# Kernel optimization log

Measured on AMD Instinct MI355X. Metric: run time of the kernel, lower is better.

Reference implementation:

```python
import jax, jax.numpy as jnp
import numpy as np

C = 256
D = C // 8  # query/key channels


def setup_inputs() -> dict:
    key = jax.random.key(0)
    ks = jax.random.split(key, 7)
    x = jax.random.normal(ks[0], (4, C, 64, 64), dtype=jnp.float32)
    s1 = 1.0 / np.sqrt(C)
    w1 = jax.random.normal(ks[1], (D, C), dtype=jnp.float32) * s1
    b1 = jax.random.normal(ks[2], (D,), dtype=jnp.float32) * 0.01
    w2 = jax.random.normal(ks[3], (D, C), dtype=jnp.float32) * s1
    b2 = jax.random.normal(ks[4], (D,), dtype=jnp.float32) * 0.01
    w3 = jax.random.normal(ks[5], (C, C), dtype=jnp.float32) * s1
    b3 = jax.random.normal(ks[6], (C,), dtype=jnp.float32) * 0.01
    return {"x": x, "w1": w1, "b1": b1, "w2": w2, "b2": b2, "w3": w3, "b3": b3}


def reference(x, w1, b1, w2, b2, w3, b3):
    B, Cc, W, H = x.shape
    N = W * H
    xf = x.reshape(B, Cc, N)  # [B, C, N] flattened spatial
    # 1x1 convs are per-pixel linear maps over channels
    q = jnp.einsum('dc,bcn->bnd', w1, xf) + b1  # [B, N, D]
    k = jnp.einsum('dc,bcn->bdn', w2, xf) + b2[:, None]  # [B, D, N]
    v = jnp.einsum('oc,bcn->bon', w3, xf) + b3[:, None]  # [B, C, N]
    energy = jnp.einsum('bnd,bdm->bnm', q, k)  # [B, N, N]
    attn = jax.nn.softmax(energy, axis=-1)
    out = jnp.einsum('bcm,bnm->bcn', v, attn)  # bmm(V, attn^T)
    out = out.reshape(B, Cc, W, H) + x
    return out
```

## Files before the change

### kernel.cpp

```cpp
#include <hip/hip_runtime.h>
#include <hip/hip_fp16.h>

typedef _Float16 half8 __attribute__((ext_vector_type(8)));
typedef _Float16 half2v __attribute__((ext_vector_type(2)));
typedef float f32x16 __attribute__((ext_vector_type(16)));
typedef float f32x4v __attribute__((ext_vector_type(4)));

#define MFMA16(A, B, C) __builtin_amdgcn_mfma_f32_32x32x16_f16((A), (B), (C), 0, 0, 0)

__device__ __forceinline__ f32x16 fzero16() {
  f32x16 z;
#pragma unroll
  for (int i = 0; i < 16; ++i) z[i] = 0.0f;
  return z;
}

__global__ __launch_bounds__(256) void wprep_kernel(
    const float* __restrict__ w1, const float* __restrict__ w2,
    const float* __restrict__ w3,
    _Float16* __restrict__ w1p, _Float16* __restrict__ w2p,
    _Float16* __restrict__ w3p)
{
  const int t = threadIdx.x;
  const int blk = blockIdx.x;
  if (blk < 8) {
    const int cot = blk;
    for (int e = t; e < 8192; e += 256) {
      const int j = e & 7, l = (e >> 3) & 63, cs = e >> 9;
      const int lr = l & 31, h = l >> 5;
      const int row = cot * 32 + lr;
      const int col = cs * 16 + 4 * h + (j & 3) + 8 * (j >> 2);
      w3p[((cot * 16 + cs) * 64 + l) * 8 + j] = (_Float16)w3[row * 256 + col];
    }
  } else {
    for (int e = t; e < 8192; e += 256) {
      const int j = e & 7, l = (e >> 3) & 63, cs = e >> 9;
      const int lr = l & 31, h = l >> 5;
      const int col = cs * 16 + 4 * h + (j & 3) + 8 * (j >> 2);
      const int idx = (cs * 64 + l) * 8 + j;
      w1p[idx] = (_Float16)w1[lr * 256 + col];
      w2p[idx] = (_Float16)w2[lr * 256 + col];
    }
  }
}

__global__ __launch_bounds__(256) void qkv_proj_kernel(
    const float* __restrict__ x,
    const _Float16* __restrict__ w1p, const float* __restrict__ b1,
    const _Float16* __restrict__ w2p, const float* __restrict__ b2,
    const _Float16* __restrict__ w3p, const float* __restrict__ b3,
    _Float16* __restrict__ qb, _Float16* __restrict__ kb,
    _Float16* __restrict__ vb)
{
  __shared__ f32x4v red[4][2][4][64];
  const int t = threadIdx.x, w = t >> 6, l = t & 63;
  const int lr = l & 31, h = l >> 5;
  const int b = blockIdx.x >> 7;
  const int nt = blockIdx.x & 127;
  const float* xb = x + (size_t)b * 256 * 4096 + nt * 32 + lr;
  const int cot0 = w * 2, cot1 = w * 2 + 1;

  f32x16 accq = fzero16(), acck = fzero16();
  f32x16 accv0 = fzero16(), accv1 = fzero16();

  for (int cs = 0; cs < 16; ++cs) {
    const int c0 = cs * 16 + 4 * h;
    half8 xh;
#pragma unroll
    for (int j = 0; j < 8; ++j) {
      const int c = c0 + (j & 3) + 8 * (j >> 2);
      xh[j] = (_Float16)xb[(size_t)c * 4096];
    }
    const half8 wh0 = *(const half8*)&w3p[((cot0 * 16 + cs) * 64 + l) * 8];
    const half8 wh1 = *(const half8*)&w3p[((cot1 * 16 + cs) * 64 + l) * 8];
    accv0 = MFMA16(xh, wh0, accv0);
    accv1 = MFMA16(xh, wh1, accv1);
    if ((cs >> 2) == w) {
      const half8 w1h = *(const half8*)&w1p[(cs * 64 + l) * 8];
      const half8 w2h = *(const half8*)&w2p[(cs * 64 + l) * 8];
      accq = MFMA16(w1h, xh, accq);
      acck = MFMA16(w2h, xh, acck);
    }
  }

  const float bv0 = b3[cot0 * 32 + lr];
  const float bv1 = b3[cot1 * 32 + lr];
#pragma unroll
  for (int hfq = 0; hfq < 2; ++hfq) {
    half8 p0, p1;
#pragma unroll
    for (int j = 0; j < 8; ++j) {
      p0[j] = (_Float16)(accv0[8 * hfq + j] + bv0);
      p1[j] = (_Float16)(accv1[8 * hfq + j] + bv1);
    }
    const int ms = nt * 2 + hfq;
    *(half8*)&vb[((((size_t)b * 256 + ms) * 8 + cot0) * 64 + l) * 8] = p0;
    *(half8*)&vb[((((size_t)b * 256 + ms) * 8 + cot1) * 64 + l) * 8] = p1;
  }

#pragma unroll
  for (int i4 = 0; i4 < 4; ++i4) {
    f32x4v q4, k4;
#pragma unroll
    for (int c = 0; c < 4; ++c) { q4[c] = accq[4 * i4 + c]; k4[c] = acck[4 * i4 + c]; }
    red[w][0][i4][l] = q4;
    red[w][1][i4][l] = k4;
  }
  __syncthreads();
  if (w < 2) {
    _Float16* dst = (w == 0) ? qb : kb;
    const float* bias = (w == 0) ? b1 : b2;
    f32x16 tot;
#pragma unroll
    for (int i4 = 0; i4 < 4; ++i4) {
      f32x4v v = red[0][w][i4][l];
      v += red[1][w][i4][l];
      v += red[2][w][i4][l];
      v += red[3][w][i4][l];
#pragma unroll
      for (int c = 0; c < 4; ++c) tot[4 * i4 + c] = v[c];
    }
#pragma unroll
    for (int ds = 0; ds < 2; ++ds) {
      half8 ph;
#pragma unroll
      for (int j = 0; j < 8; ++j) {
        const int d = 16 * ds + 4 * h + (j & 3) + 8 * (j >> 2);
        ph[j] = (_Float16)(tot[8 * ds + j] + bias[d]);
      }
      *(half8*)&dst[((((size_t)b * 128 + nt) * 2 + ds) * 64 + l) * 8] = ph;
    }
  }
}

__device__ __forceinline__ float max16(float vm, const f32x16& s) {
  const float g1 = fmaxf(fmaxf(s[0], s[1]), s[2]);
  const float g2 = fmaxf(fmaxf(s[3], s[4]), s[5]);
  const float g3 = fmaxf(fmaxf(s[6], s[7]), s[8]);
  const float g4 = fmaxf(fmaxf(s[9], s[10]), s[11]);
  const float g5 = fmaxf(fmaxf(s[12], s[13]), s[14]);
  const float h1 = fmaxf(fmaxf(g1, g2), g3);
  const float h2 = fmaxf(fmaxf(g4, g5), s[15]);
  return fmaxf(fmaxf(vm, h1), h2);
}

__global__ __launch_bounds__(512) void rowmax_kernel(
    const _Float16* __restrict__ qb, const _Float16* __restrict__ kb,
    float* __restrict__ Mrow)
{
  __shared__ float red[2][8][32];
  const int t = threadIdx.x, w = t >> 6, l = t & 63;
  const int bid = blockIdx.x;
  const int xcd = bid & 7;
  const int b = xcd >> 1;
  const int sp = ((bid >> 3) << 1) | (xcd & 1);
  const int sl0 = sp * 2, sl1 = sp * 2 + 1;
  const _Float16* qp0 = qb + ((((size_t)b * 128 + sl0) * 2) * 64 + l) * 8;
  const _Float16* qp1 = qb + ((((size_t)b * 128 + sl1) * 2) * 64 + l) * 8;
  const half8 q00 = *(const half8*)qp0;
  const half8 q01 = *(const half8*)(qp0 + 512);
  const half8 q10 = *(const half8*)qp1;
  const half8 q11 = *(const half8*)(qp1 + 512);
  float vm0 = -3.0e38f, vm1 = -3.0e38f;
  for (int mt = w * 16; mt < w * 16 + 16; ++mt) {
    const _Float16* kp = kb + ((((size_t)b * 128 + mt) * 2) * 64 + l) * 8;
    const half8 k0 = *(const half8*)kp;
    const half8 k1 = *(const half8*)(kp + 512);
    f32x16 s0 = fzero16();
    s0 = MFMA16(k0, q00, s0);
    s0 = MFMA16(k1, q01, s0);
    f32x16 s1 = fzero16();
    s1 = MFMA16(k0, q10, s1);
    s1 = MFMA16(k1, q11, s1);
    vm0 = max16(vm0, s0);
    vm1 = max16(vm1, s1);
  }
  vm0 = fmaxf(vm0, __shfl_xor(vm0, 32));
  vm1 = fmaxf(vm1, __shfl_xor(vm1, 32));
  if (l < 32) { red[0][w][l] = vm0; red[1][w][l] = vm1; }
  __syncthreads();
  if (t < 64) {
    const int slab = t >> 5, r = t & 31;
    float m = red[slab][0][r];
#pragma unroll
    for (int ww = 1; ww < 8; ++ww) m = fmaxf(m, red[slab][ww][r]);
    Mrow[(size_t)b * 4096 + (sp * 2 + slab) * 32 + r] = m;
  }
}

__global__ __launch_bounds__(512, 1) void attn_kernel(
    const _Float16* __restrict__ qb, const _Float16* __restrict__ kb,
    const _Float16* __restrict__ vb, const float* __restrict__ Mrow,
    const float* __restrict__ x, float* __restrict__ out)
{
  __shared__ __align__(16) _Float16 Plds[2][2][2][8][64][8];
  __shared__ float Lred[2][4][32];
  const int t = threadIdx.x, w = t >> 6, l = t & 63;
  const int lr = l & 31, h = l >> 5;
  const int bid = blockIdx.x;
  const int xcd = bid & 7;
  const int b = xcd >> 1;
  const int rg = ((bid >> 3) << 1) | (xcd & 1);
  const int sw = w >> 2;
  const int kq = w & 3;

  const _Float16* kbase = kb + (size_t)b * 131072 + (size_t)l * 8;
  const _Float16* vbase = vb + (size_t)b * 1048576 + (size_t)w * 512 + (size_t)l * 8;

#define KF(kt, ds) (*(const half8*)(kbase + ((size_t)(((kt) * 4 + kq) * 2 + (ds))) * 512))
#define VF(kt, ks) (*(const half8*)(vbase + ((size_t)(((kt) * 8 + (ks)) * 8)) * 512))

  const int rt32q = rg * 2 + sw;
  const _Float16* qp = qb + (((size_t)b * 128 + rt32q) * 2 * 64 + l) * 8;
  const half8 qf0 = *(const half8*)qp;
  const half8 qf1 = *(const half8*)(qp + 512);
  const float LOG2E = 1.44269504088896340736f;
  const float Mr = Mrow[(size_t)b * 4096 + rt32q * 32 + lr];
  const float nM2 = -Mr * LOG2E;

  f32x16 acc0 = fzero16(), acc1 = fzero16();
  float Lacc = 0.f;
  half8 va0[8], va1[8];
  half8 ka0, ka1, kb0_, kb1_;

#define EXPPACK(S, BUF, TI)                                                    \
  {                                                                            \
    float pvv[16];                                                             \
    float ls = 0.f;                                                            \
    _Pragma("unroll") for (int i = 0; i < 16; ++i) {                           \
      pvv[i] = exp2f(fmaf((S)[i], LOG2E, nM2)); ls += pvv[i];                  \
    }                                                                          \
    Lacc += ls;                                                                \
    union { half8 v; half2v h2[4]; } u0, u1;                                   \
    _Pragma("unroll") for (int jj = 0; jj < 4; ++jj) {                         \
      auto a0 = __builtin_amdgcn_cvt_pkrtz(pvv[2 * jj], pvv[2 * jj + 1]);      \
      auto a1 = __builtin_amdgcn_cvt_pkrtz(pvv[8 + 2 * jj], pvv[8 + 2 * jj + 1]); \
      u0.h2[jj] = *(half2v*)&a0;                                               \
      u1.h2[jj] = *(half2v*)&a1;                                               \
    }                                                                          \
    *(half8*)&Plds[BUF][TI][sw][kq * 2 + 0][l][0] = u0.v;                      \
    *(half8*)&Plds[BUF][TI][sw][kq * 2 + 1][l][0] = u1.v;                      \
  }

#define PVC(CB, TI, VA)                                                        \
  {                                                                            \
    __builtin_amdgcn_s_setprio(1);                                             \
    _Pragma("unroll") for (int ks = 0; ks < 8; ++ks) {                         \
      const half8 pb0 = *(const half8*)&Plds[CB][TI][0][ks][l][0];             \
      const half8 pb1 = *(const half8*)&Plds[CB][TI][1][ks][l][0];             \
      acc0 = MFMA16(VA[ks], pb0, acc0);                                        \
      acc1 = MFMA16(VA[ks], pb1, acc1);                                        \
    }                                                                          \
    __builtin_amdgcn_s_setprio(0);                                             \
  }

#pragma unroll
  for (int ks = 0; ks < 8; ++ks) va0[ks] = VF(0, ks);
#pragma unroll
  for (int ks = 0; ks < 8; ++ks) va1[ks] = VF(1, ks);
  {
    const half8 k00 = KF(0, 0), k01 = KF(0, 1);
    f32x16 s = fzero16();
    s = MFMA16(k00, qf0, s);
    s = MFMA16(k01, qf1, s);
    ka0 = KF(2, 0); ka1 = KF(2, 1);
    EXPPACK(s, 0, 0)
  }
  {
    const half8 k10 = KF(1, 0), k11 = KF(1, 1);
    f32x16 s = fzero16();
    s = MFMA16(k10, qf0, s);
    s = MFMA16(k11, qf1, s);
    kb0_ = KF(3, 0); kb1_ = KF(3, 1);
    EXPPACK(s, 0, 1)
  }
  asm volatile("s_waitcnt lgkmcnt(0)" ::: "memory");
  __builtin_amdgcn_s_barrier();
  asm volatile("" ::: "memory");

  for (int P = 0; P < 16; ++P) {
    const int CB = P & 1, PB = CB ^ 1;
    const int p0 = 2 * P + 2, p1 = 2 * P + 3;

    if (p0 < 32) {
      f32x16 s = fzero16();
      s = MFMA16(ka0, qf0, s);
      s = MFMA16(ka1, qf1, s);
      if (p0 + 2 < 32) { ka0 = KF(p0 + 2, 0); ka1 = KF(p0 + 2, 1); }
      EXPPACK(s, PB, 0)
    }
    PVC(CB, 0, va0)
    if (p0 < 32) {
#pragma unroll
      for (int ks = 0; ks < 8; ++ks) va0[ks] = VF(p0, ks);
    }

    if (p1 < 32) {
      f32x16 s = fzero16();
      s = MFMA16(kb0_, qf0, s);
      s = MFMA16(kb1_, qf1, s);
      if (p1 + 2 < 32) { kb0_ = KF(p1 + 2, 0); kb1_ = KF(p1 + 2, 1); }
      EXPPACK(s, PB, 1)
    }
    PVC(CB, 1, va1)
    if (p1 < 32) {
#pragma unroll
      for (int ks = 0; ks < 8; ++ks) va1[ks] = VF(p1, ks);
    }

    asm volatile("s_waitcnt lgkmcnt(0)" ::: "memory");
    __builtin_amdgcn_s_barrier();
    asm volatile("" ::: "memory");
  }
#undef PVC
#undef EXPPACK
#undef KF
#undef VF

  {
    const float l2 = Lacc + __shfl_xor(Lacc, 32);
    if (l < 32) Lred[sw][kq][lr] = l2;
  }
  __syncthreads();
  const float invL0 = 1.0f / (Lred[0][0][lr] + Lred[0][1][lr] + Lred[0][2][lr] + Lred[0][3][lr]);
  const float invL1 = 1.0f / (Lred[1][0][lr] + Lred[1][1][lr] + Lred[1][2][lr] + Lred[1][3][lr]);

  const float* xb = x + (size_t)b * 1048576;
  float* ob = out + (size_t)b * 1048576;
  const int nn0 = rg * 64 + lr;
  const int nn1 = rg * 64 + 32 + lr;
#pragma unroll
  for (int reg = 0; reg < 16; ++reg) {
    const int crel = (reg & 3) + 8 * (reg >> 2) + 4 * h;
    const int cout = w * 32 + crel;
    const size_t o0 = (size_t)cout * 4096 + nn0;
    ob[o0] = acc0[reg] * invL0 + xb[o0];
    const size_t o1 = (size_t)cout * 4096 + nn1;
    ob[o1] = acc1[reg] * invL1 + xb[o1];
  }
}

extern "C" void kernel_launch(void* const* d_in, const int* in_sizes, int n_in,
                              void* d_out, int out_size, void* d_ws, size_t ws_size,
                              hipStream_t stream) {
  const float* x  = (const float*)d_in[0];
  const float* w1 = (const float*)d_in[1];
  const float* b1 = (const float*)d_in[2];
  const float* w2 = (const float*)d_in[3];
  const float* b2 = (const float*)d_in[4];
  const float* w3 = (const float*)d_in[5];
  const float* b3 = (const float*)d_in[6];
  float* out = (float*)d_out;

  char* ws = (char*)d_ws;
  _Float16* qb  = (_Float16*)(ws);
  _Float16* kb  = (_Float16*)(ws + (1u << 20));
  _Float16* vb  = (_Float16*)(ws + (2u << 20));
  float*    Mrow = (float*)(ws + (10u << 20));
  _Float16* w1p = (_Float16*)(ws + (10u << 20) + (64u << 10));
  _Float16* w2p = (_Float16*)(ws + (10u << 20) + (96u << 10));
  _Float16* w3p = (_Float16*)(ws + (10u << 20) + (128u << 10));

  hipLaunchKernelGGL(wprep_kernel, dim3(9), dim3(256), 0, stream,
                     w1, w2, w3, w1p, w2p, w3p);
  hipLaunchKernelGGL(qkv_proj_kernel, dim3(512), dim3(256), 0, stream,
                     x, w1p, b1, w2p, b2, w3p, b3, qb, kb, vb);
  hipLaunchKernelGGL(rowmax_kernel, dim3(256), dim3(512), 0, stream, qb, kb, Mrow);
  hipLaunchKernelGGL(attn_kernel, dim3(256), dim3(512), 0, stream,
                     qb, kb, vb, Mrow, x, out);
}
```

Baseline: 74.21 us.

## Split PV key tiles across wave groups with 64-channel waves and LDS reduction

Each wave now computes 64 output channels on half of the key tiles (selected by wave group g) instead of 32 channels on every key tile. This halves the LDS reads of P per MFMA, because each P fragment feeds two channel blocks. The two partial accumulators are then summed through LDS before the final normalisation and residual add. In exchange it doubles the V register buffers and accumulators, which raises VGPR pressure, and adds an extra LDS reduction and barrier in the epilogue.

```diff
diff --git a/kernel.cpp b/kernel.cpp
--- a/kernel.cpp
+++ b/kernel.cpp
@@ -201,16 +201,17 @@
   const int xcd = bid & 7;
   const int b = xcd >> 1;
   const int rg = ((bid >> 3) << 1) | (xcd & 1);
-  const int sw = w >> 2;
+  const int g = w >> 2;
   const int kq = w & 3;
+  const int c2 = w & 3;
 
   const _Float16* kbase = kb + (size_t)b * 131072 + (size_t)l * 8;
-  const _Float16* vbase = vb + (size_t)b * 1048576 + (size_t)w * 512 + (size_t)l * 8;
+  const _Float16* vbase = vb + (size_t)b * 1048576 + (size_t)(c2 * 2) * 512 + (size_t)l * 8;
 
 #define KF(kt, ds) (*(const half8*)(kbase + ((size_t)(((kt) * 4 + kq) * 2 + (ds))) * 512))
-#define VF(kt, ks) (*(const half8*)(vbase + ((size_t)(((kt) * 8 + (ks)) * 8)) * 512))
-
-  const int rt32q = rg * 2 + sw;
+#define VF(kt, ks, ci) (*(const half8*)(vbase + ((size_t)(((kt) * 8 + (ks)) * 8 + (ci))) * 512))
+
+  const int rt32q = rg * 2 + g;
   const _Float16* qp = qb + (((size_t)b * 128 + rt32q) * 2 * 64 + l) * 8;
   const half8 qf0 = *(const half8*)qp;
   const half8 qf1 = *(const half8*)(qp + 512);
@@ -218,9 +219,9 @@
   const float Mr = Mrow[(size_t)b * 4096 + rt32q * 32 + lr];
   const float nM2 = -Mr * LOG2E;
 
-  f32x16 acc0 = fzero16(), acc1 = fzero16();
+  f32x16 a00 = fzero16(), a01 = fzero16(), a10 = fzero16(), a11 = fzero16();
   float Lacc = 0.f;
-  half8 va0[8], va1[8];
+  half8 vA[16], vB[16];
   half8 ka0, ka1, kb0_, kb1_;
 
 #define EXPPACK(S, BUF, TI)                                                    \
@@ -233,31 +234,62 @@
     Lacc += ls;                                                                \
     union { half8 v; half2v h2[4]; } u0, u1;                                   \
     _Pragma("unroll") for (int jj = 0; jj < 4; ++jj) {                         \
-      auto a0 = __builtin_amdgcn_cvt_pkrtz(pvv[2 * jj], pvv[2 * jj + 1]);      \
-      auto a1 = __builtin_amdgcn_cvt_pkrtz(pvv[8 + 2 * jj], pvv[8 + 2 * jj + 1]); \
-      u0.h2[jj] = *(half2v*)&a0;                                               \
-      u1.h2[jj] = *(half2v*)&a1;                                               \
-    }                                                                          \
-    *(half8*)&Plds[BUF][TI][sw][kq * 2 + 0][l][0] = u0.v;                      \
-    *(half8*)&Plds[BUF][TI][sw][kq * 2 + 1][l][0] = u1.v;                      \
-  }
-
-#define PVC(CB, TI, VA)                                                        \
+      auto q0 = __builtin_amdgcn_cvt_pkrtz(pvv[2 * jj], pvv[2 * jj + 1]);      \
+      auto q1 = __builtin_amdgcn_cvt_pkrtz(pvv[8 + 2 * jj], pvv[8 + 2 * jj + 1]); \
+      u0.h2[jj] = *(half2v*)&q0;                                               \
+      u1.h2[jj] = *(half2v*)&q1;                                               \
+    }                                                                          \
+    *(half8*)&Plds[BUF][TI][g][kq * 2 + 0][l][0] = u0.v;                       \
+    *(half8*)&Plds[BUF][TI][g][kq * 2 + 1][l][0] = u1.v;                       \
+  }
+
+#define PVC(CB, VA)                                                            \
   {                                                                            \
     __builtin_amdgcn_s_setprio(1);                                             \
     _Pragma("unroll") for (int ks = 0; ks < 8; ++ks) {                         \
-      const half8 pb0 = *(const half8*)&Plds[CB][TI][0][ks][l][0];             \
-      const half8 pb1 = *(const half8*)&Plds[CB][TI][1][ks][l][0];             \
-      acc0 = MFMA16(VA[ks], pb0, acc0);                                        \
-      acc1 = MFMA16(VA[ks], pb1, acc1);                                        \
+      const half8 pb0 = *(const half8*)&Plds[CB][g][0][ks][l][0];              \
+      const half8 pb1 = *(const half8*)&Plds[CB][g][1][ks][l][0];              \
+      a00 = MFMA16(VA[ks], pb0, a00);                                          \
+      a01 = MFMA16(VA[8 + ks], pb0, a01);                                      \
+      a10 = MFMA16(VA[ks], pb1, a10);                                          \
+      a11 = MFMA16(VA[8 + ks], pb1, a11);                                      \
     }                                                                          \
     __builtin_amdgcn_s_setprio(0);                                             \
   }
 
-#pragma unroll
-  for (int ks = 0; ks < 8; ++ks) va0[ks] = VF(0, ks);
-#pragma unroll
-  for (int ks = 0; ks < 8; ++ks) va1[ks] = VF(1, ks);
+#define BODY(P, VC, VN)                                                        \
+  {                                                                            \
+    const int CBv = (P) & 1, PBv = CBv ^ 1;                                    \
+    const int Tv = 2 * (P) + g;                                                \
+    const int p0 = 2 * (P) + 2, p1 = 2 * (P) + 3;                              \
+    if (Tv + 2 < 32) {                                                         \
+      _Pragma("unroll") for (int ks = 0; ks < 8; ++ks) {                       \
+        VN[ks] = VF(Tv + 2, ks, 0);                                            \
+        VN[8 + ks] = VF(Tv + 2, ks, 1);                                        \
+      }                                                                        \
+    }                                                                          \
+    if (p0 < 32) {                                                             \
+      f32x16 s = fzero16();                                                    \
+      s = MFMA16(ka0, qf0, s);                                                 \
+      s = MFMA16(ka1, qf1, s);                                                 \
+      if (p0 + 2 < 32) { ka0 = KF(p0 + 2, 0); ka1 = KF(p0 + 2, 1); }           \
+      EXPPACK(s, PBv, 0)                                                       \
+    }                                                                          \
+    PVC(CBv, VC)                                                               \
+    if (p1 < 32) {                                                             \
+      f32x16 s = fzero16();                                                    \
+      s = MFMA16(kb0_, qf0, s);                                                \
+      s = MFMA16(kb1_, qf1, s);                                                \
+      if (p1 + 2 < 32) { kb0_ = KF(p1 + 2, 0); kb1_ = KF(p1 + 2, 1); }         \
+      EXPPACK(s, PBv, 1)                                                       \
+    }                                                                          \
+    asm volatile("s_waitcnt lgkmcnt(0)" ::: "memory");                         \
+    __builtin_amdgcn_s_barrier();                                              \
+    asm volatile("" ::: "memory");                                             \
+  }
+
+#pragma unroll
+  for (int ks = 0; ks < 8; ++ks) { vA[ks] = VF(g, ks, 0); vA[8 + ks] = VF(g, ks, 1); }
   {
     const half8 k00 = KF(0, 0), k01 = KF(0, 1);
     f32x16 s = fzero16();
@@ -278,40 +310,11 @@
   __builtin_amdgcn_s_barrier();
   asm volatile("" ::: "memory");
 
-  for (int P = 0; P < 16; ++P) {
-    const int CB = P & 1, PB = CB ^ 1;
-    const int p0 = 2 * P + 2, p1 = 2 * P + 3;
-
-    if (p0 < 32) {
-      f32x16 s = fzero16();
-      s = MFMA16(ka0, qf0, s);
-      s = MFMA16(ka1, qf1, s);
-      if (p0 + 2 < 32) { ka0 = KF(p0 + 2, 0); ka1 = KF(p0 + 2, 1); }
-      EXPPACK(s, PB, 0)
-    }
-    PVC(CB, 0, va0)
-    if (p0 < 32) {
-#pragma unroll
-      for (int ks = 0; ks < 8; ++ks) va0[ks] = VF(p0, ks);
-    }
-
-    if (p1 < 32) {
-      f32x16 s = fzero16();
-      s = MFMA16(kb0_, qf0, s);
-      s = MFMA16(kb1_, qf1, s);
-      if (p1 + 2 < 32) { kb0_ = KF(p1 + 2, 0); kb1_ = KF(p1 + 2, 1); }
-      EXPPACK(s, PB, 1)
-    }
-    PVC(CB, 1, va1)
-    if (p1 < 32) {
-#pragma unroll
-      for (int ks = 0; ks < 8; ++ks) va1[ks] = VF(p1, ks);
-    }
-
-    asm volatile("s_waitcnt lgkmcnt(0)" ::: "memory");
-    __builtin_amdgcn_s_barrier();
-    asm volatile("" ::: "memory");
-  }
+  for (int PP = 0; PP < 16; PP += 2) {
+    BODY(PP, vA, vB)
+    BODY(PP + 1, vB, vA)
+  }
+#undef BODY
 #undef PVC
 #undef EXPPACK
 #undef KF
@@ -319,24 +322,51 @@
 
   {
     const float l2 = Lacc + __shfl_xor(Lacc, 32);
-    if (l < 32) Lred[sw][kq][lr] = l2;
+    if (l < 32) Lred[g][kq][lr] = l2;
   }
   __syncthreads();
-  const float invL0 = 1.0f / (Lred[0][0][lr] + Lred[0][1][lr] + Lred[0][2][lr] + Lred[0][3][lr]);
-  const float invL1 = 1.0f / (Lred[1][0][lr] + Lred[1][1][lr] + Lred[1][2][lr] + Lred[1][3][lr]);
-
-  const float* xb = x + (size_t)b * 1048576;
-  float* ob = out + (size_t)b * 1048576;
-  const int nn0 = rg * 64 + lr;
-  const int nn1 = rg * 64 + 32 + lr;
-#pragma unroll
-  for (int reg = 0; reg < 16; ++reg) {
-    const int crel = (reg & 3) + 8 * (reg >> 2) + 4 * h;
-    const int cout = w * 32 + crel;
-    const size_t o0 = (size_t)cout * 4096 + nn0;
-    ob[o0] = acc0[reg] * invL0 + xb[o0];
-    const size_t o1 = (size_t)cout * 4096 + nn1;
-    ob[o1] = acc1[reg] * invL1 + xb[o1];
+
+  float* fl = (float*)&Plds[0][0][0][0][0][0];
+  if (g == 0) {
+#pragma unroll
+    for (int j = 0; j < 4; ++j) {
+      const f32x16 av = (j == 0) ? a00 : (j == 1) ? a01 : (j == 2) ? a10 : a11;
+#pragma unroll
+      for (int reg = 0; reg < 16; ++reg)
+        fl[((w * 4 + j) * 16 + reg) * 64 + l] = av[reg];
+    }
+  }
+  __syncthreads();
+  if (g == 1) {
+    const int pw = w - 4;
+#pragma unroll
+    for (int reg = 0; reg < 16; ++reg) {
+      a00[reg] += fl[((pw * 4 + 0) * 16 + reg) * 64 + l];
+      a01[reg] += fl[((pw * 4 + 1) * 16 + reg) * 64 + l];
+      a10[reg] += fl[((pw * 4 + 2) * 16 + reg) * 64 + l];
+      a11[reg] += fl[((pw * 4 + 3) * 16 + reg) * 64 + l];
+    }
+    const float invL0 = 1.0f / (Lred[0][0][lr] + Lred[0][1][lr] + Lred[0][2][lr] + Lred[0][3][lr]);
+    const float invL1 = 1.0f / (Lred[1][0][lr] + Lred[1][1][lr] + Lred[1][2][lr] + Lred[1][3][lr]);
+
+    const float* xb = x + (size_t)b * 1048576;
+    float* ob = out + (size_t)b * 1048576;
+    const int nn0 = rg * 64 + lr;
+    const int nn1 = rg * 64 + 32 + lr;
+#pragma unroll
+    for (int reg = 0; reg < 16; ++reg) {
+      const int crel = (reg & 3) + 8 * (reg >> 2) + 4 * h;
+      const int cout0 = (c2 * 2 + 0) * 32 + crel;
+      const int cout1 = (c2 * 2 + 1) * 32 + crel;
+      const size_t o00 = (size_t)cout0 * 4096 + nn0;
+      ob[o00] = a00[reg] * invL0 + xb[o00];
+      const size_t o01 = (size_t)cout1 * 4096 + nn0;
+      ob[o01] = a01[reg] * invL0 + xb[o01];
+      const size_t o10 = (size_t)cout0 * 4096 + nn1;
+      ob[o10] = a10[reg] * invL1 + xb[o10];
+      const size_t o11 = (size_t)cout1 * 4096 + nn1;
+      ob[o11] = a11[reg] * invL1 + xb[o11];
+    }
   }
 }
 
```

Result: slower. 99.05 us (+33.5%).

## Fuse row-max pass into attention kernel and widen weight-prep grid

Applied to the files above, without the earlier changes.

Removes the separate rowmax kernel and its Mrow round-trip. Each attention block now computes the per-row max itself, with each wave scanning a quarter of the keys and reducing through shared memory, before the exp/PV pipeline. The V prefetch is moved ahead of the max pass so those loads overlap it. The weight-prep kernel is split across 40 blocks instead of 9 to shorten its critical path. The trade-off is a second pass over K inside the attention kernel plus two extra block barriers, in exchange for one fewer launch and dependency.

```diff
diff --git a/kernel.cpp b/kernel.cpp
--- a/kernel.cpp
+++ b/kernel.cpp
@@ -13,6 +13,17 @@
 #pragma unroll
   for (int i = 0; i < 16; ++i) z[i] = 0.0f;
   return z;
+}
+
+__device__ __forceinline__ float max16(float vm, const f32x16& s) {
+  const float g1 = fmaxf(fmaxf(s[0], s[1]), s[2]);
+  const float g2 = fmaxf(fmaxf(s[3], s[4]), s[5]);
+  const float g3 = fmaxf(fmaxf(s[6], s[7]), s[8]);
+  const float g4 = fmaxf(fmaxf(s[9], s[10]), s[11]);
+  const float g5 = fmaxf(fmaxf(s[12], s[13]), s[14]);
+  const float h1 = fmaxf(fmaxf(g1, g2), g3);
+  const float h2 = fmaxf(fmaxf(g4, g5), s[15]);
+  return fmaxf(fmaxf(vm, h1), h2);
 }
 
 __global__ __launch_bounds__(256) void wprep_kernel(
@@ -23,9 +34,9 @@
 {
   const int t = threadIdx.x;
   const int blk = blockIdx.x;
-  if (blk < 8) {
-    const int cot = blk;
-    for (int e = t; e < 8192; e += 256) {
+  if (blk < 32) {
+    const int cot = blk >> 2, sub = blk & 3;
+    for (int e = sub * 2048 + t; e < sub * 2048 + 2048; e += 256) {
       const int j = e & 7, l = (e >> 3) & 63, cs = e >> 9;
       const int lr = l & 31, h = l >> 5;
       const int row = cot * 32 + lr;
@@ -33,7 +44,8 @@
       w3p[((cot * 16 + cs) * 64 + l) * 8 + j] = (_Float16)w3[row * 256 + col];
     }
   } else {
-    for (int e = t; e < 8192; e += 256) {
+    const int sub = blk - 32;
+    for (int e = sub * 1024 + t; e < sub * 1024 + 1024; e += 256) {
       const int j = e & 7, l = (e >> 3) & 63, cs = e >> 9;
       const int lr = l & 31, h = l >> 5;
       const int col = cs * 16 + 4 * h + (j & 3) + 8 * (j >> 2);
@@ -133,64 +145,9 @@
   }
 }
 
-__device__ __forceinline__ float max16(float vm, const f32x16& s) {
-  const float g1 = fmaxf(fmaxf(s[0], s[1]), s[2]);
-  const float g2 = fmaxf(fmaxf(s[3], s[4]), s[5]);
-  const float g3 = fmaxf(fmaxf(s[6], s[7]), s[8]);
-  const float g4 = fmaxf(fmaxf(s[9], s[10]), s[11]);
-  const float g5 = fmaxf(fmaxf(s[12], s[13]), s[14]);
-  const float h1 = fmaxf(fmaxf(g1, g2), g3);
-  const float h2 = fmaxf(fmaxf(g4, g5), s[15]);
-  return fmaxf(fmaxf(vm, h1), h2);
-}
-
-__global__ __launch_bounds__(512) void rowmax_kernel(
-    const _Float16* __restrict__ qb, const _Float16* __restrict__ kb,
-    float* __restrict__ Mrow)
-{
-  __shared__ float red[2][8][32];
-  const int t = threadIdx.x, w = t >> 6, l = t & 63;
-  const int bid = blockIdx.x;
-  const int xcd = bid & 7;
-  const int b = xcd >> 1;
-  const int sp = ((bid >> 3) << 1) | (xcd & 1);
-  const int sl0 = sp * 2, sl1 = sp * 2 + 1;
-  const _Float16* qp0 = qb + ((((size_t)b * 128 + sl0) * 2) * 64 + l) * 8;
-  const _Float16* qp1 = qb + ((((size_t)b * 128 + sl1) * 2) * 64 + l) * 8;
-  const half8 q00 = *(const half8*)qp0;
-  const half8 q01 = *(const half8*)(qp0 + 512);
-  const half8 q10 = *(const half8*)qp1;
-  const half8 q11 = *(const half8*)(qp1 + 512);
-  float vm0 = -3.0e38f, vm1 = -3.0e38f;
-  for (int mt = w * 16; mt < w * 16 + 16; ++mt) {
-    const _Float16* kp = kb + ((((size_t)b * 128 + mt) * 2) * 64 + l) * 8;
-    const half8 k0 = *(const half8*)kp;
-    const half8 k1 = *(const half8*)(kp + 512);
-    f32x16 s0 = fzero16();
-    s0 = MFMA16(k0, q00, s0);
-    s0 = MFMA16(k1, q01, s0);
-    f32x16 s1 = fzero16();
-    s1 = MFMA16(k0, q10, s1);
-    s1 = MFMA16(k1, q11, s1);
-    vm0 = max16(vm0, s0);
-    vm1 = max16(vm1, s1);
-  }
-  vm0 = fmaxf(vm0, __shfl_xor(vm0, 32));
-  vm1 = fmaxf(vm1, __shfl_xor(vm1, 32));
-  if (l < 32) { red[0][w][l] = vm0; red[1][w][l] = vm1; }
-  __syncthreads();
-  if (t < 64) {
-    const int slab = t >> 5, r = t & 31;
-    float m = red[slab][0][r];
-#pragma unroll
-    for (int ww = 1; ww < 8; ++ww) m = fmaxf(m, red[slab][ww][r]);
-    Mrow[(size_t)b * 4096 + (sp * 2 + slab) * 32 + r] = m;
-  }
-}
-
 __global__ __launch_bounds__(512, 1) void attn_kernel(
     const _Float16* __restrict__ qb, const _Float16* __restrict__ kb,
-    const _Float16* __restrict__ vb, const float* __restrict__ Mrow,
+    const _Float16* __restrict__ vb,
     const float* __restrict__ x, float* __restrict__ out)
 {
   __shared__ __align__(16) _Float16 Plds[2][2][2][8][64][8];
@@ -208,6 +165,7 @@
   const _Float16* vbase = vb + (size_t)b * 1048576 + (size_t)w * 512 + (size_t)l * 8;
 
 #define KF(kt, ds) (*(const half8*)(kbase + ((size_t)(((kt) * 4 + kq) * 2 + (ds))) * 512))
+#define KFM(m, ds) (*(const half8*)(kbase + ((size_t)((m) * 2 + (ds))) * 512))
 #define VF(kt, ks) (*(const half8*)(vbase + ((size_t)(((kt) * 8 + (ks)) * 8)) * 512))
 
   const int rt32q = rg * 2 + sw;
@@ -215,13 +173,35 @@
   const half8 qf0 = *(const half8*)qp;
   const half8 qf1 = *(const half8*)(qp + 512);
   const float LOG2E = 1.44269504088896340736f;
-  const float Mr = Mrow[(size_t)b * 4096 + rt32q * 32 + lr];
-  const float nM2 = -Mr * LOG2E;
 
   f32x16 acc0 = fzero16(), acc1 = fzero16();
   float Lacc = 0.f;
   half8 va0[8], va1[8];
   half8 ka0, ka1, kb0_, kb1_;
+
+#pragma unroll
+  for (int ks = 0; ks < 8; ++ks) va0[ks] = VF(0, ks);
+#pragma unroll
+  for (int ks = 0; ks < 8; ++ks) va1[ks] = VF(1, ks);
+
+  {
+    float vm = -3.0e38f;
+    for (int m = kq * 32; m < kq * 32 + 32; ++m) {
+      const half8 k0 = KFM(m, 0);
+      const half8 k1 = KFM(m, 1);
+      f32x16 s = fzero16();
+      s = MFMA16(k0, qf0, s);
+      s = MFMA16(k1, qf1, s);
+      vm = max16(vm, s);
+    }
+    vm = fmaxf(vm, __shfl_xor(vm, 32));
+    if (l < 32) Lred[sw][kq][lr] = vm;
+  }
+  __syncthreads();
+  const float Mr = fmaxf(fmaxf(Lred[sw][0][lr], Lred[sw][1][lr]),
+                         fmaxf(Lred[sw][2][lr], Lred[sw][3][lr]));
+  const float nM2 = -Mr * LOG2E;
+  __syncthreads();
 
 #define EXPPACK(S, BUF, TI)                                                    \
   {                                                                            \
@@ -254,10 +234,6 @@
     __builtin_amdgcn_s_setprio(0);                                             \
   }
 
-#pragma unroll
-  for (int ks = 0; ks < 8; ++ks) va0[ks] = VF(0, ks);
-#pragma unroll
-  for (int ks = 0; ks < 8; ++ks) va1[ks] = VF(1, ks);
   {
     const half8 k00 = KF(0, 0), k01 = KF(0, 1);
     f32x16 s = fzero16();
@@ -315,6 +291,7 @@
 #undef PVC
 #undef EXPPACK
 #undef KF
+#undef KFM
 #undef VF
 
   {
@@ -356,16 +333,14 @@
   _Float16* qb  = (_Float16*)(ws);
   _Float16* kb  = (_Float16*)(ws + (1u << 20));
   _Float16* vb  = (_Float16*)(ws + (2u << 20));
-  float*    Mrow = (float*)(ws + (10u << 20));
   _Float16* w1p = (_Float16*)(ws + (10u << 20) + (64u << 10));
   _Float16* w2p = (_Float16*)(ws + (10u << 20) + (96u << 10));
   _Float16* w3p = (_Float16*)(ws + (10u << 20) + (128u << 10));
 
-  hipLaunchKernelGGL(wprep_kernel, dim3(9), dim3(256), 0, stream,
+  hipLaunchKernelGGL(wprep_kernel, dim3(40), dim3(256), 0, stream,
                      w1, w2, w3, w1p, w2p, w3p);
   hipLaunchKernelGGL(qkv_proj_kernel, dim3(512), dim3(256), 0, stream,
                      x, w1p, b1, w2p, b2, w3p, b3, qb, kb, vb);
-  hipLaunchKernelGGL(rowmax_kernel, dim3(256), dim3(512), 0, stream, qb, kb, Mrow);
   hipLaunchKernelGGL(attn_kernel, dim3(256), dim3(512), 0, stream,
-                     qb, kb, vb, Mrow, x, out);
-}
+                     qb, kb, vb, x, out);
+}
```

New measurement: 76.22 us. +2.7%, slower.
